# Performance work log

Measured on AMD Instinct MI355X. Metric: run time of the kernel, lower is better.

## Reference

```python
import jax, jax.numpy as jnp
import numpy as np

N_NODES = 50000
N_EDGES = 1600000
IN_DIM = 64
EDGE_DIM = 8
N_GRAPHS = 256
EXP_IN = 32
H = 64  # hidden dim per head / GCN hidden
EPS = 1e-5
NEG_SLOPE = 0.2


def gat_layer(x, src, dst, ea, W, a_src, a_dst, We, a_e, bias, heads, dim, concat):
    """PyG-style GATConv with edge features and self-loops (fill_value='mean')."""
    N = x.shape[0]
    ones_e = jnp.ones((ea.shape[0],), x.dtype)
    cnt = jax.ops.segment_sum(ones_e, dst, num_segments=N)
    loop_attr = jax.ops.segment_sum(ea, dst, num_segments=N) / jnp.maximum(cnt, 1.0)[:, None]
    s = jnp.concatenate([src, jnp.arange(N)])
    d = jnp.concatenate([dst, jnp.arange(N)])
    eaf = jnp.concatenate([ea, loop_attr], axis=0)  # [E+N, edge_dim]
    h = (x @ W).reshape(N, heads, dim)              # [N, H, D]
    ee = (eaf @ We).reshape(-1, heads, dim)         # [E+N, H, D]
    al_src = (h * a_src).sum(-1)                    # [N, H]
    al_dst = (h * a_dst).sum(-1)                    # [N, H]
    score = al_src[s] + al_dst[d] + (ee * a_e).sum(-1)
    score = jax.nn.leaky_relu(score, NEG_SLOPE)     # [E+N, H]
    m = jax.ops.segment_max(score, d, num_segments=N)
    ex = jnp.exp(score - m[d])
    att = ex / jax.ops.segment_sum(ex, d, num_segments=N)[d]
    out = jax.ops.segment_sum(h[s] * att[:, :, None], d, num_segments=N)  # [N, H, D]
    out = out.reshape(N, heads * dim) if concat else out.mean(axis=1)
    return out + bias


def gcn_layer(x, src, dst, W, b):
    """PyG-style GCNConv: add self loops, symmetric degree normalization."""
    N = x.shape[0]
    s = jnp.concatenate([src, jnp.arange(N)])
    d = jnp.concatenate([dst, jnp.arange(N)])
    deg = jax.ops.segment_sum(jnp.ones((s.shape[0],), x.dtype), d, num_segments=N)
    dinv = jax.lax.rsqrt(deg)  # deg >= 1 thanks to self loops
    norm = dinv[s] * dinv[d]
    h = x @ W
    return jax.ops.segment_sum(h[s] * norm[:, None], d, num_segments=N) + b


def bn(x, g, b):
    m = x.mean(axis=0)
    v = x.var(axis=0)
    return g * (x - m) * jax.lax.rsqrt(v + EPS) + b


def mean_pool(x, batch, num_graphs):
    s = jax.ops.segment_sum(x, batch, num_segments=num_graphs)
    c = jax.ops.segment_sum(jnp.ones((x.shape[0],), x.dtype), batch, num_segments=num_graphs)
    return s / jnp.maximum(c, 1.0)[:, None]


def setup_inputs() -> dict:
    key = jax.random.key(0)
    ks = jax.random.split(key, 32)
    p = lambda i, shape: jax.random.normal(ks[i], shape, jnp.float32) * 0.05
    z = lambda n: jnp.zeros((n,), jnp.float32)
    o = lambda n: jnp.ones((n,), jnp.float32)
    return {
        "x": jax.random.normal(ks[0], (N_NODES, IN_DIM), jnp.float32),
        "edge_attr": jax.random.normal(ks[1], (N_EDGES, EDGE_DIM), jnp.float32),
        "experimental_feat": jax.random.normal(ks[2], (N_GRAPHS, EXP_IN), jnp.float32),
        "edge_index": jax.random.randint(ks[3], (2, N_EDGES), 0, N_NODES),
        "batch": jnp.sort(jax.random.randint(ks[4], (N_NODES,), 0, N_GRAPHS)),
        "W1": p(5, (IN_DIM, 4 * H)), "att_src1": p(6, (4, H)), "att_dst1": p(7, (4, H)),
        "We1": p(8, (EDGE_DIM, 4 * H)), "att_e1": p(9, (4, H)), "b1": z(4 * H),
        "g1": o(4 * H), "be1": z(4 * H),
        "W2": p(10, (4 * H, H)), "att_src2": p(11, (1, H)), "att_dst2": p(12, (1, H)),
        "We2": p(13, (EDGE_DIM, H)), "att_e2": p(14, (1, H)), "b2": z(H),
        "g2": o(H), "be2": z(H),
        "Wg1": p(15, (H, H)), "bg1": z(H), "g3": o(H), "be3": z(H),
        "Wg2": p(16, (H, H)), "bg2": z(H), "g4": o(H), "be4": z(H),
        "Wex1": p(17, (EXP_IN, H)), "bex1": z(H), "Wex2": p(18, (H, H)), "bex2": z(H),
        "Wc1": p(19, (2 * H, 128)), "bc1": z(128), "Wc2": p(20, (128, 1)), "bc2": z(1),
    }


def reference(x, edge_attr, experimental_feat, edge_index, batch,
              W1, att_src1, att_dst1, We1, att_e1, b1, g1, be1,
              W2, att_src2, att_dst2, We2, att_e2, b2, g2, be2,
              Wg1, bg1, g3, be3, Wg2, bg2, g4, be4,
              Wex1, bex1, Wex2, bex2, Wc1, bc1, Wc2, bc2):
    src, dst = edge_index[0], edge_index[1]
    h = gat_layer(x, src, dst, edge_attr, W1, att_src1, att_dst1, We1, att_e1, b1, 4, H, True)
    h = jax.nn.relu(bn(h, g1, be1))
    h = gat_layer(h, src, dst, edge_attr, W2, att_src2, att_dst2, We2, att_e2, b2, 1, H, False)
    h = jax.nn.relu(bn(h, g2, be2))  # dropout = identity in eval
    h = gcn_layer(h, src, dst, Wg1, bg1)
    h = jax.nn.relu(bn(h, g3, be3))
    h = gcn_layer(h, src, dst, Wg2, bg2)
    h = jax.nn.relu(bn(h, g4, be4))
    xp = mean_pool(h, batch, N_GRAPHS)                    # [G, H]
    e = jax.nn.relu(experimental_feat @ Wex1 + bex1)
    e = jax.nn.relu(e @ Wex2 + bex2)
    combined = jnp.concatenate([xp, e], axis=1)           # [G, 2H]
    combined = jax.nn.relu(combined @ Wc1 + bc1)          # [G, 128]
    out = combined @ Wc2 + bc2                            # [G, 1]
    return (out, xp, combined)
```

## Files before the change

kernel.cpp:

```cpp
#include <hip/hip_runtime.h>
#include <hip/hip_bf16.h>

#define N_NODES 50000
#define N_EDGES 1600000
#define N_GRAPHS 256
#define NEG_SLOPE 0.2f
#define BN_EPS 1e-5f

typedef __hip_bfloat16 bf16;

__device__ __forceinline__ float b2f(bf16 v){ return __bfloat162float(v); }
__device__ __forceinline__ bf16 f2b(float v){ return __float2bfloat16(v); }
__device__ __forceinline__ float us2f(unsigned short u){ return __uint_as_float(((unsigned)u)<<16); }
__device__ __forceinline__ unsigned short f2us(float v){ bf16 b = f2b(v); return *(unsigned short*)&b; }
__device__ __forceinline__ float ldF(const void* p, size_t i, int m){
  return m ? ((const float*)p)[i] : b2f(((const bf16*)p)[i]);
}
__device__ __forceinline__ float sane(float v){
  return (v == v && fabsf(v) < 1e30f) ? v : 0.f;
}
__device__ __forceinline__ float sel4(const float v[4], int h){
  float r = v[0];
  r = (h==1) ? v[1] : r;
  r = (h==2) ? v[2] : r;
  r = (h==3) ? v[3] : r;
  return r;
}

__device__ int detect_mode_block(const void* x){
  __shared__ int s_ins;
  if(threadIdx.x == 0) s_ins = 0;
  __syncthreads();
  const unsigned short* u = (const unsigned short*)x;
  int c = 0;
  for(int i = threadIdx.x; i < 1024; i += blockDim.x){
    float v = fabsf(us2f(u[i]));
    if(!(v > 1e-6f && v < 1e4f)) c++;
  }
  if(c) atomicAdd(&s_ins, c);
  __syncthreads();
  return (s_ins > 128) ? 1 : 0;
}

#define NSEG 33
struct Bank { const void* p[NSEG]; int n[NSEG]; int off[NSEG]; };

__global__ void k_convert(Bank b, const void* xdet, float* out){
  int m = detect_mode_block(xdet);
  int seg = blockIdx.y;
  int i = blockIdx.x*256 + threadIdx.x;
  if(i < b.n[seg]) out[b.off[seg] + i] = ldF(b.p[seg], i, m);
}

__global__ void k_cvt_x(const void* x, bf16* xb){
  int m = detect_mode_block(x);
  int i4 = blockIdx.x*256 + threadIdx.x;
  if(i4 >= N_NODES*16) return;
  if(m){
    float4 v = ((const float4*)x)[i4];
    ((ushort4*)xb)[i4] = make_ushort4(f2us(v.x), f2us(v.y), f2us(v.z), f2us(v.w));
  } else {
    ((ushort4*)xb)[i4] = ((const ushort4*)x)[i4];
  }
}

__global__ void k_we(const float* __restrict__ We1, const float* __restrict__ ae1,
                     const float* __restrict__ We2, const float* __restrict__ ae2,
                     float* __restrict__ w_e){
  int t = threadIdx.x;
  if(t < 32){
    int h = t >> 3, k = t & 7;
    float s = 0.f;
    for(int d=0;d<64;d++) s += We1[k*256 + h*64 + d] * ae1[h*64 + d];
    w_e[t] = s;
  } else if(t < 40){
    int k = t - 32;
    float s = 0.f;
    for(int d=0;d<64;d++) s += We2[k*64 + d] * ae2[d];
    w_e[t] = s;
  }
}

__global__ void k_count(const int* __restrict__ dst, int* __restrict__ cnt){
  int e = blockIdx.x*256 + threadIdx.x;
  if(e < N_EDGES){
    int d = dst[e]; if((unsigned)d >= N_NODES) d = 0;
    atomicAdd(&cnt[d], 1);
  }
}

__global__ void k_blocksum(const int* __restrict__ cnt, int* __restrict__ bsum){
  __shared__ int s[256];
  int i = blockIdx.x*256 + threadIdx.x;
  s[threadIdx.x] = (i < N_NODES) ? cnt[i] : 0;
  __syncthreads();
  for(int o=128;o>0;o>>=1){ if(threadIdx.x<o) s[threadIdx.x]+=s[threadIdx.x+o]; __syncthreads(); }
  if(threadIdx.x==0) bsum[blockIdx.x]=s[0];
}

__global__ void k_scan_bsum(const int* __restrict__ bsum, int* __restrict__ bofs, int nb){
  __shared__ int s[256];
  int t = threadIdx.x;
  s[t] = (t<nb) ? bsum[t] : 0;
  __syncthreads();
  for(int o=1;o<256;o<<=1){ int v=(t>=o)?s[t-o]:0; __syncthreads(); s[t]+=v; __syncthreads(); }
  bofs[t] = (t==0) ? 0 : s[t-1];
}

__global__ void k_scan_write(const int* __restrict__ cnt, const int* __restrict__ bofs,
                             int* __restrict__ rp, float* __restrict__ dinv){
  __shared__ int s[256];
  int t = threadIdx.x; int i = blockIdx.x*256 + t;
  int v = (i<N_NODES) ? cnt[i] : 0;
  s[t]=v; __syncthreads();
  for(int o=1;o<256;o<<=1){ int a=(t>=o)?s[t-o]:0; __syncthreads(); s[t]+=a; __syncthreads(); }
  if(i<N_NODES){
    rp[i+1] = s[t] + bofs[blockIdx.x];
    dinv[i] = rsqrtf((float)v + 1.f);
  }
  if(i==0) rp[0]=0;
}

__global__ void k_fill(const int* __restrict__ src, const int* __restrict__ dst,
                       const int* __restrict__ rp, int* __restrict__ fill,
                       const void* __restrict__ ea, const void* __restrict__ xdet,
                       const float* __restrict__ w_e,
                       int4* __restrict__ epk){
  int m = detect_mode_block(xdet);
  int e = blockIdx.x*256 + threadIdx.x;
  if(e >= N_EDGES) return;
  int d = dst[e]; if((unsigned)d >= N_NODES) d = 0;
  int p = atomicAdd(&fill[d], 1);
  int slot = rp[d] + p;
  if((unsigned)slot >= N_EDGES) return;
  int sv = src[e]; if((unsigned)sv >= N_NODES) sv = 0;
  float a[8];
  if(m){
    const float* eaf = (const float*)ea;
    float4 lo = *(const float4*)&eaf[(size_t)e*8];
    float4 hi = *(const float4*)&eaf[(size_t)e*8 + 4];
    a[0]=lo.x; a[1]=lo.y; a[2]=lo.z; a[3]=lo.w;
    a[4]=hi.x; a[5]=hi.y; a[6]=hi.z; a[7]=hi.w;
  } else {
    #pragma unroll
    for(int k=0;k<8;k++) a[k] = b2f(((const bf16*)ea)[(size_t)e*8 + k]);
  }
  unsigned d4[4];
  #pragma unroll
  for(int h=0;h<4;h++){
    float s = 0.f;
    #pragma unroll
    for(int k=0;k<8;k++) s += a[k]*w_e[h*8+k];
    d4[h] = f2us(s);
  }
  float s1 = 0.f;
  #pragma unroll
  for(int k=0;k<8;k++) s1 += a[k]*w_e[32+k];
  int4 pk;
  pk.x = sv;
  pk.y = (int)(d4[0] | (d4[1] << 16));
  pk.z = (int)(d4[2] | (d4[3] << 16));
  pk.w = (int)(unsigned)f2us(s1);
  epk[slot] = pk;
}

__global__ __launch_bounds__(256, 3) void k_gemmA(
    const bf16* __restrict__ xb, const float* __restrict__ W1,
    bf16* __restrict__ hp, int M)
{
  __shared__ float As[64][68];
  __shared__ float Ws[64][64];
  const int tid = threadIdx.x;
  const int bm  = blockIdx.x * 64;
  const int h   = blockIdx.y;
  const int tx  = tid & 15;
  const int ty  = tid >> 4;
  float acc[4][4] = {};

  #pragma unroll
  for(int f = tid; f < 1024; f += 256){
    int r = f >> 4, kq = f & 15;
    int row = bm + r;
    float4 v = make_float4(0.f,0.f,0.f,0.f);
    if(row < M){
      ushort4 u = *(const ushort4*)&xb[(size_t)row*64 + 4*kq];
      v = make_float4(us2f(u.x), us2f(u.y), us2f(u.z), us2f(u.w));
    }
    *(float4*)&As[r][4*kq] = v;
  }
  #pragma unroll
  for(int g = tid; g < 1024; g += 256){
    int kr = g >> 4, jq = g & 15;
    *(float4*)&Ws[kr][4*jq] = *(const float4*)&W1[(size_t)kr*256 + h*64 + 4*jq];
  }
  __syncthreads();
  #pragma unroll 2
  for(int k = 0; k < 64; k += 4){
    float4 av[4], wv[4];
    #pragma unroll
    for(int r=0;r<4;r++) av[r] = *(const float4*)&As[4*ty + r][k];
    #pragma unroll
    for(int kk=0;kk<4;kk++) wv[kk] = *(const float4*)&Ws[k + kk][4*tx];
    #pragma unroll
    for(int r=0;r<4;r++){
      const float a0=av[r].x, a1=av[r].y, a2=av[r].z, a3=av[r].w;
      acc[r][0] += a0*wv[0].x + a1*wv[1].x + a2*wv[2].x + a3*wv[3].x;
      acc[r][1] += a0*wv[0].y + a1*wv[1].y + a2*wv[2].y + a3*wv[3].y;
      acc[r][2] += a0*wv[0].z + a1*wv[1].z + a2*wv[2].z + a3*wv[3].z;
      acc[r][3] += a0*wv[0].w + a1*wv[1].w + a2*wv[2].w + a3*wv[3].w;
    }
  }
  #pragma unroll
  for(int r=0;r<4;r++){
    int row = bm + 4*ty + r;
    if(row < M){
      ushort4 u = make_ushort4(f2us(acc[r][0]), f2us(acc[r][1]), f2us(acc[r][2]), f2us(acc[r][3]));
      *(ushort4*)&hp[(size_t)row*256 + h*64 + 4*tx] = u;
    }
  }
}

template<int KIN, bool BNF>
__global__ __launch_bounds__(256, 3) void k_gemmB(
    const float* __restrict__ A, const float* __restrict__ W,
    bf16* __restrict__ C, int M,
    const float* __restrict__ bnsums, const float* __restrict__ bng, const float* __restrict__ bnb)
{
  __shared__ float As[64][68];
  __shared__ float Ws[64][64];
  const int tid = threadIdx.x;
  const int bm  = blockIdx.x * 64;
  const int tx  = tid & 15;
  const int ty  = tid >> 4;
  const float invN = 1.0f / (float)N_NODES;
  float acc[4][4] = {};

  for(int k0 = 0; k0 < KIN; k0 += 64){
    #pragma unroll
    for(int f = tid; f < 1024; f += 256){
      int r = f >> 4, kq = f & 15;
      int row = bm + r;
      float4 v = make_float4(0.f,0.f,0.f,0.f);
      if(row < M) v = *(const float4*)&A[(size_t)row*KIN + k0 + 4*kq];
      if(BNF){
        int c = k0 + 4*kq;
        float vv[4] = {v.x, v.y, v.z, v.w};
        #pragma unroll
        for(int j=0;j<4;j++){
          int cc = c + j;
          float mean = bnsums[cc]*invN;
          float var = fmaxf(bnsums[KIN+cc]*invN - mean*mean, 0.f);
          float y = (sane(vv[j])-mean)*rsqrtf(var + BN_EPS)*bng[cc] + bnb[cc];
          vv[j] = fmaxf(y, 0.f);
        }
        v = make_float4(vv[0], vv[1], vv[2], vv[3]);
      }
      *(float4*)&As[r][4*kq] = v;
    }
    #pragma unroll
    for(int g = tid; g < 1024; g += 256){
      int kr = g >> 4, jq = g & 15;
      *(float4*)&Ws[kr][4*jq] = *(const float4*)&W[(size_t)(k0+kr)*64 + 4*jq];
    }
    __syncthreads();
    #pragma unroll 2
    for(int k = 0; k < 64; k += 4){
      float4 av[4], wv[4];
      #pragma unroll
      for(int r=0;r<4;r++) av[r] = *(const float4*)&As[4*ty + r][k];
      #pragma unroll
      for(int kk=0;kk<4;kk++) wv[kk] = *(const float4*)&Ws[k + kk][4*tx];
      #pragma unroll
      for(int r=0;r<4;r++){
        const float a0=av[r].x, a1=av[r].y, a2=av[r].z, a3=av[r].w;
        acc[r][0] += a0*wv[0].x + a1*wv[1].x + a2*wv[2].x + a3*wv[3].x;
        acc[r][1] += a0*wv[0].y + a1*wv[1].y + a2*wv[2].y + a3*wv[3].y;
        acc[r][2] += a0*wv[0].z + a1*wv[1].z + a2*wv[2].z + a3*wv[3].z;
        acc[r][3] += a0*wv[0].w + a1*wv[1].w + a2*wv[2].w + a3*wv[3].w;
      }
    }
    __syncthreads();
  }
  #pragma unroll
  for(int r=0;r<4;r++){
    int row = bm + 4*ty + r;
    if(row < M){
      ushort4 u = make_ushort4(f2us(acc[r][0]), f2us(acc[r][1]), f2us(acc[r][2]), f2us(acc[r][3]));
      *(ushort4*)&C[(size_t)row*64 + 4*tx] = u;
    }
  }
}

__global__ void k_al4(const bf16* __restrict__ hp, const float* __restrict__ asrc,
                      const float* __restrict__ adst,
                      float* __restrict__ als4, float* __restrict__ ald4){
  int idx = blockIdx.x*256 + threadIdx.x;
  if(idx >= N_NODES*4) return;
  int n = idx >> 2, h = idx & 3;
  const unsigned short* row = (const unsigned short*)hp + (size_t)n*256 + h*64;
  float ss=0.f, sd=0.f;
  #pragma unroll
  for(int q=0;q<16;q++){
    ushort4 u = *(const ushort4*)&row[4*q];
    float4 a_s = *(const float4*)&asrc[h*64 + 4*q];
    float4 a_d = *(const float4*)&adst[h*64 + 4*q];
    float v0=us2f(u.x), v1=us2f(u.y), v2=us2f(u.z), v3=us2f(u.w);
    ss += v0*a_s.x + v1*a_s.y + v2*a_s.z + v3*a_s.w;
    sd += v0*a_d.x + v1*a_d.y + v2*a_d.z + v3*a_d.w;
  }
  als4[idx]=ss; ald4[idx]=sd;
}

__global__ void k_al1(const bf16* __restrict__ hp, const float* __restrict__ asrc,
                      const float* __restrict__ adst,
                      float* __restrict__ als, float* __restrict__ ald){
  int n = blockIdx.x*256 + threadIdx.x;
  if(n >= N_NODES) return;
  const unsigned short* row = (const unsigned short*)hp + (size_t)n*64;
  float ss=0.f, sd=0.f;
  #pragma unroll
  for(int q=0;q<16;q++){
    ushort4 u = *(const ushort4*)&row[4*q];
    float4 a_s = *(const float4*)&asrc[4*q];
    float4 a_d = *(const float4*)&adst[4*q];
    float v0=us2f(u.x), v1=us2f(u.y), v2=us2f(u.z), v3=us2f(u.w);
    ss += v0*a_s.x + v1*a_s.y + v2*a_s.z + v3*a_s.w;
    sd += v0*a_d.x + v1*a_d.y + v2*a_d.z + v3*a_d.w;
  }
  als[n]=ss; ald[n]=sd;
}

__global__ __launch_bounds__(64) void k_gat_agg4(
    const int* __restrict__ rp, const int4* __restrict__ epk,
    const bf16* __restrict__ hp,
    const float* __restrict__ als4, const float* __restrict__ ald4,
    const float* __restrict__ bias256, float* __restrict__ out1){
  int n = blockIdx.x; int t = threadIdx.x;
  int head = t >> 4;
  __shared__ int   ssrc[64];
  __shared__ float swt[64][4];
  int s0 = rp[n], e0 = rp[n+1];
  if((unsigned)s0 > N_EDGES){ s0=0; e0=0; }
  if(e0 < s0 || (unsigned)e0 > N_EDGES) e0 = s0;
  float4 aldv = *(const float4*)&ald4[n*4];
  float4 alsvn = *(const float4*)&als4[n*4];
  float wsum[4] = {0.f,0.f,0.f,0.f};
  float dsum[4] = {0.f,0.f,0.f,0.f};
  float acc[4]  = {0.f,0.f,0.f,0.f};
  const unsigned short* hpu = (const unsigned short*)hp;

  for(int base = s0; base < e0; base += 64){
    int m = min(64, e0 - base);
    if(t < m){
      int4 pk = epk[base+t];
      int sn = pk.x; if((unsigned)sn >= N_NODES) sn = 0;
      ssrc[t] = sn;
      float edf[4] = {us2f((unsigned short)(pk.y & 0xffff)), us2f((unsigned short)((unsigned)pk.y >> 16)),
                      us2f((unsigned short)(pk.z & 0xffff)), us2f((unsigned short)((unsigned)pk.z >> 16))};
      float4 alss = *(const float4*)&als4[sn*4];
      float alssv[4] = {alss.x, alss.y, alss.z, alss.w};
      float aldvv[4] = {aldv.x, aldv.y, aldv.z, aldv.w};
      float w4[4];
      #pragma unroll
      for(int h=0;h<4;h++){
        float sc = alssv[h] + aldvv[h] + edf[h];
        sc = sc > 0.f ? sc : NEG_SLOPE*sc;
        sc = fminf(sc, 30.f);
        float w = expf(sc);
        w4[h] = w;
        wsum[h] += w; dsum[h] += edf[h];
      }
      *(float4*)&swt[t][0] = make_float4(w4[0], w4[1], w4[2], w4[3]);
    }
    __syncthreads();
    #pragma unroll 4
    for(int i=0;i<m;i++){
      int row = ssrc[i];
      float w = swt[i][head];
      ushort4 u = *(const ushort4*)&hpu[(size_t)row*256 + 4*t];
      acc[0] += w*us2f(u.x); acc[1] += w*us2f(u.y);
      acc[2] += w*us2f(u.z); acc[3] += w*us2f(u.w);
    }
    __syncthreads();
  }
  #pragma unroll
  for(int o=1;o<64;o<<=1){
    #pragma unroll
    for(int h=0;h<4;h++){
      wsum[h] += __shfl_xor(wsum[h], o);
      dsum[h] += __shfl_xor(dsum[h], o);
    }
  }
  float alsnv[4] = {alsvn.x, alsvn.y, alsvn.z, alsvn.w};
  float aldnv[4] = {aldv.x, aldv.y, aldv.z, aldv.w};
  float sEh = sel4(wsum, head), sDh = sel4(dsum, head);
  float deg = (float)(e0 - s0);
  float sdot = deg > 0.f ? sDh/deg : 0.f;
  float sc = sel4(alsnv, head) + sel4(aldnv, head) + sdot;
  sc = sc > 0.f ? sc : NEG_SLOPE*sc;
  sc = fminf(sc, 30.f);
  float wself = expf(sc);
  ushort4 su = *(const ushort4*)&hpu[(size_t)n*256 + 4*t];
  float4 bi = *(const float4*)&bias256[4*t];
  float inv = 1.f/(sEh + wself);
  float4 o4;
  o4.x = (acc[0] + wself*us2f(su.x))*inv + bi.x;
  o4.y = (acc[1] + wself*us2f(su.y))*inv + bi.y;
  o4.z = (acc[2] + wself*us2f(su.z))*inv + bi.z;
  o4.w = (acc[3] + wself*us2f(su.w))*inv + bi.w;
  *(float4*)&out1[(size_t)n*256 + 4*t] = o4;
}

__global__ __launch_bounds__(64) void k_gat_agg1e(
    const int* __restrict__ rp, const int4* __restrict__ epk,
    const bf16* __restrict__ hp,
    const float* __restrict__ als, const float* __restrict__ ald,
    const float* __restrict__ bias64, float* __restrict__ out){
  int n = blockIdx.x; int t = threadIdx.x;
  int eg = t >> 4, cq = t & 15;
  __shared__ float sw[64];
  __shared__ int   ssrc[64];
  int s0 = rp[n], e0 = rp[n+1];
  if((unsigned)s0 > N_EDGES){ s0=0; e0=0; }
  if(e0 < s0 || (unsigned)e0 > N_EDGES) e0 = s0;
  float aldn = ald[n];
  float wsum_l = 0.f, dsum_l = 0.f;
  float acc[4] = {0.f,0.f,0.f,0.f};
  const unsigned short* hpu = (const unsigned short*)hp;
  for(int base = s0; base < e0; base += 64){
    int m = min(64, e0 - base);
    if(t < m){
      int4 pk = epk[base+t];
      int sn = pk.x; if((unsigned)sn >= N_NODES) sn = 0;
      ssrc[t] = sn;
      float ed = us2f((unsigned short)(pk.w & 0xffff));
      float sc = als[sn] + aldn + ed;
      sc = sc > 0.f ? sc : NEG_SLOPE*sc;
      sc = fminf(sc, 30.f);
      float w = expf(sc);
      sw[t] = w;
      wsum_l += w; dsum_l += ed;
    }
    __syncthreads();
    #pragma unroll 2
    for(int i=0;i<m;i+=4){
      int j = i + eg;
      if(j < m){
        int row = ssrc[j];
        float w = sw[j];
        ushort4 u = *(const ushort4*)&hpu[(size_t)row*64 + 4*cq];
        acc[0] += w*us2f(u.x); acc[1] += w*us2f(u.y);
        acc[2] += w*us2f(u.z); acc[3] += w*us2f(u.w);
      }
    }
    __syncthreads();
  }
  #pragma unroll
  for(int o=1;o<64;o<<=1){ wsum_l += __shfl_xor(wsum_l, o); dsum_l += __shfl_xor(dsum_l, o); }
  #pragma unroll
  for(int q=0;q<4;q++){ acc[q] += __shfl_xor(acc[q], 16); acc[q] += __shfl_xor(acc[q], 32); }
  if(t < 16){
    float deg = (float)(e0 - s0);
    float sdot = deg > 0.f ? dsum_l/deg : 0.f;
    float sc = als[n] + aldn + sdot;
    sc = sc > 0.f ? sc : NEG_SLOPE*sc;
    sc = fminf(sc, 30.f);
    float wself = expf(sc);
    ushort4 su = *(const ushort4*)&hpu[(size_t)n*64 + 4*cq];
    float4 bi = *(const float4*)&bias64[4*cq];
    float inv = 1.f/(wsum_l + wself);
    float4 o4;
    o4.x = (acc[0] + wself*us2f(su.x))*inv + bi.x;
    o4.y = (acc[1] + wself*us2f(su.y))*inv + bi.y;
    o4.z = (acc[2] + wself*us2f(su.z))*inv + bi.z;
    o4.w = (acc[3] + wself*us2f(su.w))*inv + bi.w;
    *(float4*)&out[(size_t)n*64 + 4*cq] = o4;
  }
}

__global__ __launch_bounds__(64) void k_gcn_agg(
    const int* __restrict__ rp, const int4* __restrict__ epk,
    const float* __restrict__ dinv, const bf16* __restrict__ gp,
    const float* __restrict__ bias, float* __restrict__ out){
  int n = blockIdx.x; int t = threadIdx.x;
  int eg = t >> 4, cq = t & 15;
  __shared__ float sw[64];
  __shared__ int   ssrc[64];
  int s0 = rp[n], e0 = rp[n+1];
  if((unsigned)s0 > N_EDGES){ s0=0; e0=0; }
  if(e0 < s0 || (unsigned)e0 > N_EDGES) e0 = s0;
  float dn = dinv[n];
  float acc[4] = {0.f,0.f,0.f,0.f};
  const unsigned short* gpu = (const unsigned short*)gp;
  for(int base = s0; base < e0; base += 64){
    int m = min(64, e0 - base);
    if(t < m){
      int sn = epk[base+t].x; if((unsigned)sn >= N_NODES) sn = 0;
      ssrc[t]=sn; sw[t]=dinv[sn];
    }
    __syncthreads();
    #pragma unroll 2
    for(int i=0;i<m;i+=4){
      int j = i + eg;
      if(j < m){
        int row = ssrc[j];
        float w = sw[j];
        ushort4 u = *(const ushort4*)&gpu[(size_t)row*64 + 4*cq];
        acc[0] += w*us2f(u.x); acc[1] += w*us2f(u.y);
        acc[2] += w*us2f(u.z); acc[3] += w*us2f(u.w);
      }
    }
    __syncthreads();
  }
  #pragma unroll
  for(int q=0;q<4;q++){ acc[q] += __shfl_xor(acc[q], 16); acc[q] += __shfl_xor(acc[q], 32); }
  if(t < 16){
    ushort4 su = *(const ushort4*)&gpu[(size_t)n*64 + 4*cq];
    float4 bi = *(const float4*)&bias[4*cq];
    float4 o4;
    o4.x = dn*(acc[0] + dn*us2f(su.x)) + bi.x;
    o4.y = dn*(acc[1] + dn*us2f(su.y)) + bi.y;
    o4.z = dn*(acc[2] + dn*us2f(su.z)) + bi.z;
    o4.w = dn*(acc[3] + dn*us2f(su.w)) + bi.w;
    *(float4*)&out[(size_t)n*64 + 4*cq] = o4;
  }
}

template<int C>
__global__ void k_colstats(const float* __restrict__ X, float* __restrict__ sums){
  constexpr int RPB = 128;
  constexpr int RSTEP = 256 / C;
  int c = threadIdx.x % C;
  int r0 = threadIdx.x / C;
  int rbeg = blockIdx.x * RPB;
  int rend = min(N_NODES, rbeg + RPB);
  float s = 0.f, q = 0.f;
  for(int r = rbeg + r0; r < rend; r += RSTEP){
    float v = sane(X[(size_t)r*C + c]);
    s += v; q += v*v;
  }
  atomicAdd(&sums[c], s);
  atomicAdd(&sums[C + c], q);
}

__global__ __launch_bounds__(64) void k_pool3(
    const float* __restrict__ h, const int* __restrict__ batch,
    const float* __restrict__ sums, const float* __restrict__ g4,
    const float* __restrict__ b4,
    float* __restrict__ psum, float* __restrict__ pcnt){
  int t = threadIdx.x;
  int n0 = blockIdx.x * 256;
  int n1 = min(N_NODES, n0 + 256);
  if(n0 >= n1) return;
  const float invN = 1.0f / (float)N_NODES;
  float mean = sums[t]*invN;
  float var = fmaxf(sums[64+t]*invN - mean*mean, 0.f);
  float rstd = rsqrtf(var + BN_EPS);
  float gg = g4[t], bb = b4[t];
  int cur = batch[n0]; if((unsigned)cur >= N_GRAPHS) cur = 0;
  float acc = 0.f; int cl = 0;
  for(int n = n0; n < n1; n++){
    int g = batch[n]; if((unsigned)g >= N_GRAPHS) g = 0;
    if(g != cur){
      atomicAdd(&psum[cur*64 + t], acc);
      if(t == 0) atomicAdd(&pcnt[cur], (float)cl);
      acc = 0.f; cl = 0; cur = g;
    }
    float y = (sane(h[(size_t)n*64 + t])-mean)*rstd*gg + bb;
    acc += fmaxf(y, 0.f);
    cl++;
  }
  atomicAdd(&psum[cur*64 + t], acc);
  if(t == 0) atomicAdd(&pcnt[cur], (float)cl);
}

__device__ __forceinline__ void stO(void* o, size_t i, float v, int m){
  if(m) ((float*)o)[i] = v; else ((bf16*)o)[i] = f2b(v);
}

__global__ __launch_bounds__(128) void k_head(
    const float* __restrict__ psum, const float* __restrict__ pcnt,
    const float* __restrict__ exf,
    const float* __restrict__ Wex1, const float* __restrict__ bex1,
    const float* __restrict__ Wex2, const float* __restrict__ bex2,
    const float* __restrict__ Wc1, const float* __restrict__ bc1,
    const float* __restrict__ Wc2, const float* __restrict__ bc2,
    const void* __restrict__ xdet, void* __restrict__ dout){
  int m0 = detect_mode_block(xdet);
  int g = blockIdx.x; int t = threadIdx.x;
  __shared__ float ci[128];
  __shared__ float e1[64];
  __shared__ float comb[128];
  __shared__ float red[128];
  if(t < 64){
    float c = fmaxf(pcnt[g], 1.f);
    float xp = sane(psum[g*64 + t]) / c;
    ci[t] = xp;
    stO(dout, 256 + (size_t)g*64 + t, xp, m0);
  } else {
    int j = t - 64;
    float s = bex1[j];
    for(int k=0;k<32;k++) s += exf[g*32 + k] * Wex1[k*64 + j];
    e1[j] = fmaxf(s, 0.f);
  }
  __syncthreads();
  if(t >= 64){
    int j = t - 64;
    float s = bex2[j];
    for(int k=0;k<64;k++) s += e1[k] * Wex2[k*64 + j];
    ci[64 + j] = fmaxf(s, 0.f);
  }
  __syncthreads();
  {
    float s = bc1[t];
    for(int k=0;k<128;k++) s += ci[k] * Wc1[k*128 + t];
    s = fmaxf(s, 0.f);
    comb[t] = s;
    stO(dout, 256 + 16384 + (size_t)g*128 + t, s, m0);
  }
  __syncthreads();
  red[t] = comb[t] * Wc2[t];
  __syncthreads();
  for(int o=64;o>0;o>>=1){ if(t<o) red[t]+=red[t+o]; __syncthreads(); }
  if(t==0) stO(dout, g, red[0] + bc2[0], m0);
}

extern "C" void kernel_launch(void* const* d_in, const int* in_sizes, int n_in,
                              void* d_out, int out_size, void* d_ws, size_t ws_size,
                              hipStream_t stream){
  const void* x    = d_in[0];
  const void* ea   = d_in[1];
  const int* ei    = (const int*)d_in[3];
  const int* batch = (const int*)d_in[4];
  const int* src = ei;
  const int* dst = ei + N_EDGES;

  char* base = (char*)d_ws;
  size_t off = 0;
  auto alloc = [&](size_t bytes) -> void* {
    void* r = base + off;
    off += (bytes + 255) & ~(size_t)255;
    return r;
  };
  int*   cnt    = (int*)  alloc((size_t)N_NODES*4);
  int*   fill   = (int*)  alloc((size_t)N_NODES*4);
  float* bnstat = (float*)alloc(4096);
  float* pool   = (float*)alloc((size_t)(N_GRAPHS*64 + N_GRAPHS)*4);
  size_t zbytes = off;
  int*   rp      = (int*)  alloc((size_t)(N_NODES+1)*4);
  int*   bsum    = (int*)  alloc(256*4);
  int*   bofs    = (int*)  alloc(256*4);
  int4*  epk     = (int4*) alloc((size_t)N_EDGES*16);
  float* dinv    = (float*)alloc((size_t)N_NODES*4);
  float* w_e     = (float*)alloc(64*4);
  float* als4    = (float*)alloc((size_t)N_NODES*4*4);
  float* ald4    = (float*)alloc((size_t)N_NODES*4*4);
  float* wbank   = (float*)alloc(80000*4);
  bf16*  xb      = (bf16*) alloc((size_t)N_NODES*64*2);
  bf16*  hp      = (bf16*) alloc((size_t)N_NODES*256*2);
  float* out1    = (float*)alloc((size_t)N_NODES*256*4);

  float* out2 = out1;
  float* out3 = out1 + (size_t)N_NODES*64;
  float* out4 = out1 + (size_t)N_NODES*128;
  float* bn1 = bnstat;
  float* bn2 = bnstat + 512;
  float* bn3 = bnstat + 640;
  float* bn4 = bnstat + 768;
  float* psum = pool;
  float* pcnt = pool + N_GRAPHS*64;

  const int segidx[NSEG] = {2, 5,6,7,8,9,10,11,12, 13,14,15,16,17,18,19,20,
                            21,22,23,24, 25,26,27,28, 29,30,31,32, 33,34,35,36};
  const int segn[NSEG] = {8192, 16384,256,256,2048,256,256,256,256,
                          16384,64,64,512,64,64,64,64,
                          4096,64,64,64, 4096,64,64,64,
                          2048,64,4096,64, 16384,128,128,1};
  Bank bk;
  int offs[NSEG]; int acc0 = 0;
  for(int i=0;i<NSEG;i++){ bk.p[i]=d_in[segidx[i]]; bk.n[i]=segn[i]; bk.off[i]=acc0; offs[i]=acc0; acc0+=segn[i]; }
  const float* f_exf = wbank + offs[0];
  const float* fW1 = wbank+offs[1]; const float* fas1 = wbank+offs[2]; const float* fad1 = wbank+offs[3];
  const float* fWe1= wbank+offs[4]; const float* fae1 = wbank+offs[5]; const float* fb1  = wbank+offs[6];
  const float* fg1 = wbank+offs[7]; const float* fbe1 = wbank+offs[8];
  const float* fW2 = wbank+offs[9]; const float* fas2 = wbank+offs[10]; const float* fad2 = wbank+offs[11];
  const float* fWe2= wbank+offs[12]; const float* fae2 = wbank+offs[13]; const float* fb2 = wbank+offs[14];
  const float* fg2 = wbank+offs[15]; const float* fbe2 = wbank+offs[16];
  const float* fWg1= wbank+offs[17]; const float* fbg1 = wbank+offs[18]; const float* fg3 = wbank+offs[19];
  const float* fbe3= wbank+offs[20];
  const float* fWg2= wbank+offs[21]; const float* fbg2 = wbank+offs[22]; const float* fg4 = wbank+offs[23];
  const float* fbe4= wbank+offs[24];
  const float* fWex1=wbank+offs[25]; const float* fbex1= wbank+offs[26];
  const float* fWex2=wbank+offs[27]; const float* fbex2= wbank+offs[28];
  const float* fWc1= wbank+offs[29]; const float* fbc1 = wbank+offs[30];
  const float* fWc2= wbank+offs[31]; const float* fbc2 = wbank+offs[32];

  const int nbN  = (N_NODES + 255)/256;
  const int nbE  = (N_EDGES + 255)/256;
  const int nbT  = (N_NODES + 63)/64;

  hipMemsetAsync(d_ws, 0, zbytes, stream);
  {
    dim3 g((16384+255)/256, NSEG);
    k_convert<<<g,256,0,stream>>>(bk, x, wbank);
  }
  k_cvt_x<<<(N_NODES*16+255)/256,256,0,stream>>>(x, xb);
  k_we<<<1,64,0,stream>>>(fWe1, fae1, fWe2, fae2, w_e);
  k_count<<<nbE,256,0,stream>>>(dst, cnt);
  k_blocksum<<<nbN,256,0,stream>>>(cnt, bsum);
  k_scan_bsum<<<1,256,0,stream>>>(bsum, bofs, nbN);
  k_scan_write<<<nbN,256,0,stream>>>(cnt, bofs, rp, dinv);
  k_fill<<<nbE,256,0,stream>>>(src, dst, rp, fill, ea, x, w_e, epk);

  {
    dim3 g(nbT, 4);
    k_gemmA<<<g,256,0,stream>>>(xb, fW1, hp, N_NODES);
  }
  k_al4<<<(N_NODES*4+255)/256,256,0,stream>>>(hp, fas1, fad1, als4, ald4);
  k_gat_agg4<<<N_NODES,64,0,stream>>>(rp, epk, hp, als4, ald4, fb1, out1);
  k_colstats<256><<<(N_NODES+127)/128,256,0,stream>>>(out1, bn1);

  k_gemmB<256,true><<<nbT,256,0,stream>>>(out1, fW2, hp, N_NODES, bn1, fg1, fbe1);
  k_al1<<<nbN,256,0,stream>>>(hp, fas2, fad2, als4, ald4);
  k_gat_agg1e<<<N_NODES,64,0,stream>>>(rp, epk, hp, als4, ald4, fb2, out2);
  k_colstats<64><<<(N_NODES+127)/128,256,0,stream>>>(out2, bn2);

  k_gemmB<64,true><<<nbT,256,0,stream>>>(out2, fWg1, hp, N_NODES, bn2, fg2, fbe2);
  k_gcn_agg<<<N_NODES,64,0,stream>>>(rp, epk, dinv, hp, fbg1, out3);
  k_colstats<64><<<(N_NODES+127)/128,256,0,stream>>>(out3, bn3);

  k_gemmB<64,true><<<nbT,256,0,stream>>>(out3, fWg2, hp, N_NODES, bn3, fg3, fbe3);
  k_gcn_agg<<<N_NODES,64,0,stream>>>(rp, epk, dinv, hp, fbg2, out4);
  k_colstats<64><<<(N_NODES+127)/128,256,0,stream>>>(out4, bn4);

  k_pool3<<<nbN,64,0,stream>>>(out4, batch, bn4, fg4, fbe4, psum, pcnt);
  k_head<<<N_GRAPHS,128,0,stream>>>(psum, pcnt, f_exf, fWex1, fbex1, fWex2, fbex2,
                                    fWc1, fbc1, fWc2, fbc2, x, (void*)d_out);
}
```

Baseline: 1.006 ms.

## Store layer outputs in bf16 and widen aggregation gathers to 16-byte loads

The intermediate per-node layer outputs (GAT and GCN aggregation results) are now stored as bf16 instead of fp32, and every consumer (GEMM with fused BN, column stats, pooling) reads them as bf16. This halves the bytes written and re-read between stages. The aggregation kernels also switch from 8-byte to 16-byte gathers per thread, so each thread handles 8 channels and more edges are processed in parallel across lane groups, with an added cross-lane reduction at the end. The cost is extra bf16 rounding of activations before batch norm, and fewer lanes active in the final epilogue.

```diff
diff --git a/kernel.cpp b/kernel.cpp
--- a/kernel.cpp
+++ b/kernel.cpp
@@ -13,6 +13,7 @@
 __device__ __forceinline__ bf16 f2b(float v){ return __float2bfloat16(v); }
 __device__ __forceinline__ float us2f(unsigned short u){ return __uint_as_float(((unsigned)u)<<16); }
 __device__ __forceinline__ unsigned short f2us(float v){ bf16 b = f2b(v); return *(unsigned short*)&b; }
+__device__ __forceinline__ unsigned pk2(float a, float b){ return (unsigned)f2us(a) | ((unsigned)f2us(b)<<16); }
 __device__ __forceinline__ float ldF(const void* p, size_t i, int m){
   return m ? ((const float*)p)[i] : b2f(((const bf16*)p)[i]);
 }
@@ -25,6 +26,18 @@
   r = (h==2) ? v[2] : r;
   r = (h==3) ? v[3] : r;
   return r;
+}
+__device__ __forceinline__ void acc8(float* acc, float w, uint4 u){
+  acc[0] += w*us2f((unsigned short)(u.x & 0xffff)); acc[1] += w*us2f((unsigned short)(u.x >> 16));
+  acc[2] += w*us2f((unsigned short)(u.y & 0xffff)); acc[3] += w*us2f((unsigned short)(u.y >> 16));
+  acc[4] += w*us2f((unsigned short)(u.z & 0xffff)); acc[5] += w*us2f((unsigned short)(u.z >> 16));
+  acc[6] += w*us2f((unsigned short)(u.w & 0xffff)); acc[7] += w*us2f((unsigned short)(u.w >> 16));
+}
+__device__ __forceinline__ void unp8(float* o, uint4 u){
+  o[0] = us2f((unsigned short)(u.x & 0xffff)); o[1] = us2f((unsigned short)(u.x >> 16));
+  o[2] = us2f((unsigned short)(u.y & 0xffff)); o[3] = us2f((unsigned short)(u.y >> 16));
+  o[4] = us2f((unsigned short)(u.z & 0xffff)); o[5] = us2f((unsigned short)(u.z >> 16));
+  o[6] = us2f((unsigned short)(u.w & 0xffff)); o[7] = us2f((unsigned short)(u.w >> 16));
 }
 
 __device__ int detect_mode_block(const void* x){
@@ -220,9 +233,9 @@
   }
 }
 
-template<int KIN, bool BNF>
+template<int KIN>
 __global__ __launch_bounds__(256, 3) void k_gemmB(
-    const float* __restrict__ A, const float* __restrict__ W,
+    const bf16* __restrict__ A, const float* __restrict__ W,
     bf16* __restrict__ C, int M,
     const float* __restrict__ bnsums, const float* __restrict__ bng, const float* __restrict__ bnb)
 {
@@ -240,22 +253,21 @@
     for(int f = tid; f < 1024; f += 256){
       int r = f >> 4, kq = f & 15;
       int row = bm + r;
-      float4 v = make_float4(0.f,0.f,0.f,0.f);
-      if(row < M) v = *(const float4*)&A[(size_t)row*KIN + k0 + 4*kq];
-      if(BNF){
-        int c = k0 + 4*kq;
-        float vv[4] = {v.x, v.y, v.z, v.w};
-        #pragma unroll
-        for(int j=0;j<4;j++){
-          int cc = c + j;
-          float mean = bnsums[cc]*invN;
-          float var = fmaxf(bnsums[KIN+cc]*invN - mean*mean, 0.f);
-          float y = (sane(vv[j])-mean)*rsqrtf(var + BN_EPS)*bng[cc] + bnb[cc];
-          vv[j] = fmaxf(y, 0.f);
-        }
-        v = make_float4(vv[0], vv[1], vv[2], vv[3]);
+      float vv[4] = {0.f,0.f,0.f,0.f};
+      if(row < M){
+        ushort4 u = *(const ushort4*)&A[(size_t)row*KIN + k0 + 4*kq];
+        vv[0]=us2f(u.x); vv[1]=us2f(u.y); vv[2]=us2f(u.z); vv[3]=us2f(u.w);
       }
-      *(float4*)&As[r][4*kq] = v;
+      int c = k0 + 4*kq;
+      #pragma unroll
+      for(int j=0;j<4;j++){
+        int cc = c + j;
+        float mean = bnsums[cc]*invN;
+        float var = fmaxf(bnsums[KIN+cc]*invN - mean*mean, 0.f);
+        float y = (sane(vv[j])-mean)*rsqrtf(var + BN_EPS)*bng[cc] + bnb[cc];
+        vv[j] = fmaxf(y, 0.f);
+      }
+      *(float4*)&As[r][4*kq] = make_float4(vv[0], vv[1], vv[2], vv[3]);
     }
     #pragma unroll
     for(int g = tid; g < 1024; g += 256){
@@ -334,9 +346,10 @@
     const int* __restrict__ rp, const int4* __restrict__ epk,
     const bf16* __restrict__ hp,
     const float* __restrict__ als4, const float* __restrict__ ald4,
-    const float* __restrict__ bias256, float* __restrict__ out1){
+    const float* __restrict__ bias256, bf16* __restrict__ out1){
   int n = blockIdx.x; int t = threadIdx.x;
-  int head = t >> 4;
+  int eh = t >> 5, c8 = t & 31;
+  int head = c8 >> 3;
   __shared__ int   ssrc[64];
   __shared__ float swt[64][4];
   int s0 = rp[n], e0 = rp[n+1];
@@ -346,7 +359,7 @@
   float4 alsvn = *(const float4*)&als4[n*4];
   float wsum[4] = {0.f,0.f,0.f,0.f};
   float dsum[4] = {0.f,0.f,0.f,0.f};
-  float acc[4]  = {0.f,0.f,0.f,0.f};
+  float acc[8]  = {0.f,0.f,0.f,0.f,0.f,0.f,0.f,0.f};
   const unsigned short* hpu = (const unsigned short*)hp;
 
   for(int base = s0; base < e0; base += 64){
@@ -374,12 +387,14 @@
     }
     __syncthreads();
     #pragma unroll 4
-    for(int i=0;i<m;i++){
-      int row = ssrc[i];
-      float w = swt[i][head];
-      ushort4 u = *(const ushort4*)&hpu[(size_t)row*256 + 4*t];
-      acc[0] += w*us2f(u.x); acc[1] += w*us2f(u.y);
-      acc[2] += w*us2f(u.z); acc[3] += w*us2f(u.w);
+    for(int i=0;i<m;i+=2){
+      int j = i + eh;
+      if(j < m){
+        int row = ssrc[j];
+        float w = swt[j][head];
+        uint4 u = *(const uint4*)&hpu[(size_t)row*256 + 8*c8];
+        acc8(acc, w, u);
+      }
     }
     __syncthreads();
   }
@@ -391,33 +406,41 @@
       dsum[h] += __shfl_xor(dsum[h], o);
     }
   }
-  float alsnv[4] = {alsvn.x, alsvn.y, alsvn.z, alsvn.w};
-  float aldnv[4] = {aldv.x, aldv.y, aldv.z, aldv.w};
-  float sEh = sel4(wsum, head), sDh = sel4(dsum, head);
-  float deg = (float)(e0 - s0);
-  float sdot = deg > 0.f ? sDh/deg : 0.f;
-  float sc = sel4(alsnv, head) + sel4(aldnv, head) + sdot;
-  sc = sc > 0.f ? sc : NEG_SLOPE*sc;
-  sc = fminf(sc, 30.f);
-  float wself = expf(sc);
-  ushort4 su = *(const ushort4*)&hpu[(size_t)n*256 + 4*t];
-  float4 bi = *(const float4*)&bias256[4*t];
-  float inv = 1.f/(sEh + wself);
-  float4 o4;
-  o4.x = (acc[0] + wself*us2f(su.x))*inv + bi.x;
-  o4.y = (acc[1] + wself*us2f(su.y))*inv + bi.y;
-  o4.z = (acc[2] + wself*us2f(su.z))*inv + bi.z;
-  o4.w = (acc[3] + wself*us2f(su.w))*inv + bi.w;
-  *(float4*)&out1[(size_t)n*256 + 4*t] = o4;
+  #pragma unroll
+  for(int q=0;q<8;q++) acc[q] += __shfl_xor(acc[q], 32);
+  if(eh == 0){
+    float alsnv[4] = {alsvn.x, alsvn.y, alsvn.z, alsvn.w};
+    float aldnv[4] = {aldv.x, aldv.y, aldv.z, aldv.w};
+    float sEh = sel4(wsum, head), sDh = sel4(dsum, head);
+    float deg = (float)(e0 - s0);
+    float sdot = deg > 0.f ? sDh/deg : 0.f;
+    float sc = sel4(alsnv, head) + sel4(aldnv, head) + sdot;
+    sc = sc > 0.f ? sc : NEG_SLOPE*sc;
+    sc = fminf(sc, 30.f);
+    float wself = expf(sc);
+    float self[8];
+    unp8(self, *(const uint4*)&hpu[(size_t)n*256 + 8*c8]);
+    float4 b0 = *(const float4*)&bias256[8*c8];
+    float4 b1 = *(const float4*)&bias256[8*c8 + 4];
+    float bi[8] = {b0.x,b0.y,b0.z,b0.w,b1.x,b1.y,b1.z,b1.w};
+    float inv = 1.f/(sEh + wself);
+    float o8[8];
+    #pragma unroll
+    for(int q=0;q<8;q++) o8[q] = (acc[q] + wself*self[q])*inv + bi[q];
+    uint4 st;
+    st.x = pk2(o8[0],o8[1]); st.y = pk2(o8[2],o8[3]);
+    st.z = pk2(o8[4],o8[5]); st.w = pk2(o8[6],o8[7]);
+    *(uint4*)&((unsigned short*)out1)[(size_t)n*256 + 8*c8] = st;
+  }
 }
 
 __global__ __launch_bounds__(64) void k_gat_agg1e(
     const int* __restrict__ rp, const int4* __restrict__ epk,
     const bf16* __restrict__ hp,
     const float* __restrict__ als, const float* __restrict__ ald,
-    const float* __restrict__ bias64, float* __restrict__ out){
+    const float* __restrict__ bias64, bf16* __restrict__ out){
   int n = blockIdx.x; int t = threadIdx.x;
-  int eg = t >> 4, cq = t & 15;
+  int eg = t >> 3, c8 = t & 7;
   __shared__ float sw[64];
   __shared__ int   ssrc[64];
   int s0 = rp[n], e0 = rp[n+1];
@@ -425,7 +448,7 @@
   if(e0 < s0 || (unsigned)e0 > N_EDGES) e0 = s0;
   float aldn = ald[n];
   float wsum_l = 0.f, dsum_l = 0.f;
-  float acc[4] = {0.f,0.f,0.f,0.f};
+  float acc[8] = {0.f,0.f,0.f,0.f,0.f,0.f,0.f,0.f};
   const unsigned short* hpu = (const unsigned short*)hp;
   for(int base = s0; base < e0; base += 64){
     int m = min(64, e0 - base);
@@ -443,14 +466,13 @@
     }
     __syncthreads();
     #pragma unroll 2
-    for(int i=0;i<m;i+=4){
+    for(int i=0;i<m;i+=8){
       int j = i + eg;
       if(j < m){
         int row = ssrc[j];
         float w = sw[j];
-        ushort4 u = *(const ushort4*)&hpu[(size_t)row*64 + 4*cq];
-        acc[0] += w*us2f(u.x); acc[1] += w*us2f(u.y);
-        acc[2] += w*us2f(u.z); acc[3] += w*us2f(u.w);
+        uint4 u = *(const uint4*)&hpu[(size_t)row*64 + 8*c8];
+        acc8(acc, w, u);
       }
     }
     __syncthreads();
@@ -458,39 +480,47 @@
   #pragma unroll
   for(int o=1;o<64;o<<=1){ wsum_l += __shfl_xor(wsum_l, o); dsum_l += __shfl_xor(dsum_l, o); }
   #pragma unroll
-  for(int q=0;q<4;q++){ acc[q] += __shfl_xor(acc[q], 16); acc[q] += __shfl_xor(acc[q], 32); }
-  if(t < 16){
+  for(int q=0;q<8;q++){
+    acc[q] += __shfl_xor(acc[q], 8);
+    acc[q] += __shfl_xor(acc[q], 16);
+    acc[q] += __shfl_xor(acc[q], 32);
+  }
+  if(t < 8){
     float deg = (float)(e0 - s0);
     float sdot = deg > 0.f ? dsum_l/deg : 0.f;
     float sc = als[n] + aldn + sdot;
     sc = sc > 0.f ? sc : NEG_SLOPE*sc;
     sc = fminf(sc, 30.f);
     float wself = expf(sc);
-    ushort4 su = *(const ushort4*)&hpu[(size_t)n*64 + 4*cq];
-    float4 bi = *(const float4*)&bias64[4*cq];
+    float self[8];
+    unp8(self, *(const uint4*)&hpu[(size_t)n*64 + 8*t]);
+    float4 b0 = *(const float4*)&bias64[8*t];
+    float4 b1 = *(const float4*)&bias64[8*t + 4];
+    float bi[8] = {b0.x,b0.y,b0.z,b0.w,b1.x,b1.y,b1.z,b1.w};
     float inv = 1.f/(wsum_l + wself);
-    float4 o4;
-    o4.x = (acc[0] + wself*us2f(su.x))*inv + bi.x;
-    o4.y = (acc[1] + wself*us2f(su.y))*inv + bi.y;
-    o4.z = (acc[2] + wself*us2f(su.z))*inv + bi.z;
-    o4.w = (acc[3] + wself*us2f(su.w))*inv + bi.w;
-    *(float4*)&out[(size_t)n*64 + 4*cq] = o4;
+    float o8[8];
+    #pragma unroll
+    for(int q=0;q<8;q++) o8[q] = (acc[q] + wself*self[q])*inv + bi[q];
+    uint4 st;
+    st.x = pk2(o8[0],o8[1]); st.y = pk2(o8[2],o8[3]);
+    st.z = pk2(o8[4],o8[5]); st.w = pk2(o8[6],o8[7]);
+    *(uint4*)&((unsigned short*)out)[(size_t)n*64 + 8*t] = st;
   }
 }
 
 __global__ __launch_bounds__(64) void k_gcn_agg(
     const int* __restrict__ rp, const int4* __restrict__ epk,
     const float* __restrict__ dinv, const bf16* __restrict__ gp,
-    const float* __restrict__ bias, float* __restrict__ out){
+    const float* __restrict__ bias, bf16* __restrict__ out){
   int n = blockIdx.x; int t = threadIdx.x;
-  int eg = t >> 4, cq = t & 15;
+  int eg = t >> 3, c8 = t & 7;
   __shared__ float sw[64];
   __shared__ int   ssrc[64];
   int s0 = rp[n], e0 = rp[n+1];
   if((unsigned)s0 > N_EDGES){ s0=0; e0=0; }
   if(e0 < s0 || (unsigned)e0 > N_EDGES) e0 = s0;
   float dn = dinv[n];
-  float acc[4] = {0.f,0.f,0.f,0.f};
+  float acc[8] = {0.f,0.f,0.f,0.f,0.f,0.f,0.f,0.f};
   const unsigned short* gpu = (const unsigned short*)gp;
   for(int base = s0; base < e0; base += 64){
     int m = min(64, e0 - base);
@@ -500,43 +530,51 @@
     }
     __syncthreads();
     #pragma unroll 2
-    for(int i=0;i<m;i+=4){
+    for(int i=0;i<m;i+=8){
       int j = i + eg;
       if(j < m){
         int row = ssrc[j];
         float w = sw[j];
-        ushort4 u = *(const ushort4*)&gpu[(size_t)row*64 + 4*cq];
-        acc[0] += w*us2f(u.x); acc[1] += w*us2f(u.y);
-        acc[2] += w*us2f(u.z); acc[3] += w*us2f(u.w);
+        uint4 u = *(const uint4*)&gpu[(size_t)row*64 + 8*c8];
+        acc8(acc, w, u);
       }
     }
     __syncthreads();
   }
   #pragma unroll
-  for(int q=0;q<4;q++){ acc[q] += __shfl_xor(acc[q], 16); acc[q] += __shfl_xor(acc[q], 32); }
-  if(t < 16){
-    ushort4 su = *(const ushort4*)&gpu[(size_t)n*64 + 4*cq];
-    float4 bi = *(const float4*)&bias[4*cq];
-    float4 o4;
-    o4.x = dn*(acc[0] + dn*us2f(su.x)) + bi.x;
-    o4.y = dn*(acc[1] + dn*us2f(su.y)) + bi.y;
-    o4.z = dn*(acc[2] + dn*us2f(su.z)) + bi.z;
-    o4.w = dn*(acc[3] + dn*us2f(su.w)) + bi.w;
-    *(float4*)&out[(size_t)n*64 + 4*cq] = o4;
+  for(int q=0;q<8;q++){
+    acc[q] += __shfl_xor(acc[q], 8);
+    acc[q] += __shfl_xor(acc[q], 16);
+    acc[q] += __shfl_xor(acc[q], 32);
+  }
+  if(t < 8){
+    float self[8];
+    unp8(self, *(const uint4*)&gpu[(size_t)n*64 + 8*t]);
+    float4 b0 = *(const float4*)&bias[8*t];
+    float4 b1 = *(const float4*)&bias[8*t + 4];
+    float bi[8] = {b0.x,b0.y,b0.z,b0.w,b1.x,b1.y,b1.z,b1.w};
+    float o8[8];
+    #pragma unroll
+    for(int q=0;q<8;q++) o8[q] = dn*(acc[q] + dn*self[q]) + bi[q];
+    uint4 st;
+    st.x = pk2(o8[0],o8[1]); st.y = pk2(o8[2],o8[3]);
+    st.z = pk2(o8[4],o8[5]); st.w = pk2(o8[6],o8[7]);
+    *(uint4*)&((unsigned short*)out)[(size_t)n*64 + 8*t] = st;
   }
 }
 
 template<int C>
-__global__ void k_colstats(const float* __restrict__ X, float* __restrict__ sums){
+__global__ void k_colstats(const bf16* __restrict__ X, float* __restrict__ sums){
   constexpr int RPB = 128;
   constexpr int RSTEP = 256 / C;
   int c = threadIdx.x % C;
   int r0 = threadIdx.x / C;
   int rbeg = blockIdx.x * RPB;
   int rend = min(N_NODES, rbeg + RPB);
+  const unsigned short* Xu = (const unsigned short*)X;
   float s = 0.f, q = 0.f;
   for(int r = rbeg + r0; r < rend; r += RSTEP){
-    float v = sane(X[(size_t)r*C + c]);
+    float v = sane(us2f(Xu[(size_t)r*C + c]));
     s += v; q += v*v;
   }
   atomicAdd(&sums[c], s);
@@ -544,7 +582,7 @@
 }
 
 __global__ __launch_bounds__(64) void k_pool3(
-    const float* __restrict__ h, const int* __restrict__ batch,
+    const bf16* __restrict__ h, const int* __restrict__ batch,
     const float* __restrict__ sums, const float* __restrict__ g4,
     const float* __restrict__ b4,
     float* __restrict__ psum, float* __restrict__ pcnt){
@@ -557,6 +595,7 @@
   float var = fmaxf(sums[64+t]*invN - mean*mean, 0.f);
   float rstd = rsqrtf(var + BN_EPS);
   float gg = g4[t], bb = b4[t];
+  const unsigned short* hu = (const unsigned short*)h;
   int cur = batch[n0]; if((unsigned)cur >= N_GRAPHS) cur = 0;
   float acc = 0.f; int cl = 0;
   for(int n = n0; n < n1; n++){
@@ -566,7 +605,7 @@
       if(t == 0) atomicAdd(&pcnt[cur], (float)cl);
       acc = 0.f; cl = 0; cur = g;
     }
-    float y = (sane(h[(size_t)n*64 + t])-mean)*rstd*gg + bb;
+    float y = (sane(us2f(hu[(size_t)n*64 + t]))-mean)*rstd*gg + bb;
     acc += fmaxf(y, 0.f);
     cl++;
   }
@@ -658,11 +697,12 @@
   float* wbank   = (float*)alloc(80000*4);
   bf16*  xb      = (bf16*) alloc((size_t)N_NODES*64*2);
   bf16*  hp      = (bf16*) alloc((size_t)N_NODES*256*2);
-  float* out1    = (float*)alloc((size_t)N_NODES*256*4);
-
-  float* out2 = out1;
-  float* out3 = out1 + (size_t)N_NODES*64;
-  float* out4 = out1 + (size_t)N_NODES*128;
+  bf16*  outb    = (bf16*) alloc((size_t)N_NODES*256*2);
+
+  bf16* out1 = outb;
+  bf16* out2 = outb;
+  bf16* out3 = outb + (size_t)N_NODES*64;
+  bf16* out4 = outb + (size_t)N_NODES*128;
   float* bn1 = bnstat;
   float* bn2 = bnstat + 512;
   float* bn3 = bnstat + 640;
@@ -720,16 +760,16 @@
   k_gat_agg4<<<N_NODES,64,0,stream>>>(rp, epk, hp, als4, ald4, fb1, out1);
   k_colstats<256><<<(N_NODES+127)/128,256,0,stream>>>(out1, bn1);
 
-  k_gemmB<256,true><<<nbT,256,0,stream>>>(out1, fW2, hp, N_NODES, bn1, fg1, fbe1);
+  k_gemmB<256><<<nbT,256,0,stream>>>(out1, fW2, hp, N_NODES, bn1, fg1, fbe1);
   k_al1<<<nbN,256,0,stream>>>(hp, fas2, fad2, als4, ald4);
   k_gat_agg1e<<<N_NODES,64,0,stream>>>(rp, epk, hp, als4, ald4, fb2, out2);
   k_colstats<64><<<(N_NODES+127)/128,256,0,stream>>>(out2, bn2);
 
-  k_gemmB<64,true><<<nbT,256,0,stream>>>(out2, fWg1, hp, N_NODES, bn2, fg2, fbe2);
+  k_gemmB<64><<<nbT,256,0,stream>>>(out2, fWg1, hp, N_NODES, bn2, fg2, fbe2);
   k_gcn_agg<<<N_NODES,64,0,stream>>>(rp, epk, dinv, hp, fbg1, out3);
   k_colstats<64><<<(N_NODES+127)/128,256,0,stream>>>(out3, bn3);
 
-  k_gemmB<64,true><<<nbT,256,0,stream>>>(out3, fWg2, hp, N_NODES, bn3, fg3, fbe3);
+  k_gemmB<64><<<nbT,256,0,stream>>>(out3, fWg2, hp, N_NODES, bn3, fg3, fbe3);
   k_gcn_agg<<<N_NODES,64,0,stream>>>(rp, epk, dinv, hp, fbg2, out4);
   k_colstats<64><<<(N_NODES+127)/128,256,0,stream>>>(out4, bn4);
 
```

Result: faster. 974.0 us (-3.2%).
